# Kernel optimization log

Hardware: AMD Instinct MI355X
Metric: run time of the kernel (lower is better)

The kernel has to match this reference:

```python
import jax, jax.numpy as jnp
import numpy as np

B, L, H, HEADS, N_NODE = 1024, 200, 128, 8, 200000
MAXN = L + 1  # max_n_node
D = H // HEADS
EPS = 1e-12


def setup_inputs() -> dict:
    key = jax.random.key(0)
    ks = jax.random.split(key, 20)
    lengths = jax.random.randint(ks[0], (B,), 1, L + 1)
    mask = (jnp.arange(L)[None, :] < lengths[:, None]).astype(jnp.int32)  # contiguous 1s
    alias_inputs = jax.random.randint(ks[1], (B, L), 0, MAXN)
    items = jax.random.randint(ks[2], (B, MAXN), 0, N_NODE)

    def lin_w(k, o, i):
        return (jax.random.normal(k, (o, i), jnp.float32) * 0.1)

    inp = dict(
        alias_inputs=alias_inputs,
        items=items,
        mask=mask,
        emb_W=jax.random.normal(ks[3], (N_NODE, H), jnp.float32) * 0.1,
        # LastAttenion params
        W0=lin_w(ks[4], H, H), b0=jax.random.normal(ks[5], (H,), jnp.float32) * 0.1,
        W1=lin_w(ks[6], H, H), b1=jax.random.normal(ks[7], (H,), jnp.float32) * 0.1,
        W2=lin_w(ks[8], H, H), b2=jax.random.normal(ks[9], (H,), jnp.float32) * 0.1,
        # linear_q[0] (last_k = 1)
        Wq=lin_w(ks[10], H, H), bq=jax.random.normal(ks[11], (H,), jnp.float32) * 0.1,
        # linear_transform (2H -> H)
        Wt=lin_w(ks[12], H, 2 * H), bt=jax.random.normal(ks[13], (H,), jnp.float32) * 0.1,
        ln_g=jax.random.normal(ks[14], (H,), jnp.float32) * 0.1,
        ln_b=jax.random.normal(ks[15], (H,), jnp.float32) * 0.1,
    )
    return inp


def reference(alias_inputs, items, mask, emb_W, W0, b0, W1, b1, W2, b2, Wq, bq, Wt, bt, ln_g, ln_b):
    maskf = mask.astype(jnp.float32)
    # hidden = normalize(embedding(items)); dropout off (eval)
    hidden = emb_W[items]                                                  # [B, MAXN, H]
    hidden = hidden / (jnp.linalg.norm(hidden, axis=-1, keepdims=True) + EPS)
    # per-batch gather: seq_hidden[b, t] = hidden[b, alias_inputs[b, t]]
    seq = jnp.take_along_axis(hidden, alias_inputs[..., None], axis=1)     # [B, L, H]
    seq = seq * maskf[..., None]
    seq = seq / (jnp.linalg.norm(seq, axis=-1, keepdims=True) + EPS)
    # compute_scores
    lengths = mask.sum(1)
    last_idx = lengths - 1                                                 # >= 0 (lengths >= 1)
    ht_last = seq[jnp.arange(B), last_idx]                                 # [B, H]  (ht0 too)
    hts = (ht_last @ Wq.T + bq)[:, None, :]                                # [B, 1, H]
    # torch.norm over dim=1 (size 1) == elementwise abs
    hts = hts / (jnp.linalg.norm(hts, axis=1, keepdims=True) + EPS)
    # LastAttenion (last_k = 1, no lp-pool, eval dropout off)
    q0 = (hts @ W0.T + b0).reshape(B * HEADS, 1, D)                        # [B*h, 1, d]
    q1 = (seq @ W1.T + b1).reshape(B * HEADS, L, D)                        # [B*h, L, d]
    q2 = (seq @ W2.T + b2).reshape(B, L, HEADS, D)                         # [B, L, h, d]
    alpha = jax.nn.sigmoid(jnp.einsum('bkd,bld->bkl', q0, q1))             # [B*h, 1, L]
    alpha = alpha.reshape(B, HEADS, L).transpose(0, 2, 1)                  # [B, L, h]
    alpha = jax.nn.softmax(2.0 * alpha, axis=1)
    a = jnp.sum((alpha[..., None] * q2).reshape(B, L, H) * maskf[..., None], axis=1)  # [B, H]
    # layernorm eps=1e-8
    mu = a.mean(-1, keepdims=True)
    var = ((a - mu) ** 2).mean(-1, keepdims=True)
    a = (a - mu) / jnp.sqrt(var + 1e-8) * ln_g + ln_b
    a = jnp.concatenate([a, ht_last], axis=1) @ Wt.T + bt                  # [B, H]
    # norm=True branch
    a = a / (jnp.linalg.norm(a, axis=1, keepdims=True) + EPS)
    b = emb_W[1:]
    b = b / (jnp.linalg.norm(b, axis=1, keepdims=True) + EPS)
    return a, b.T                                                          # [B,H], [H, N_NODE-1]
```

## Files before the change

### kernel.cpp

```cpp
#include <hip/hip_runtime.h>
#include <math.h>

typedef unsigned int uint;
typedef unsigned short ushort;

__device__ __forceinline__ float b2f(ushort u){
  union { uint i; float f; } v; v.i = ((uint)u) << 16; return v.f;
}
__device__ __forceinline__ ushort f2b(float f){
  union { float f; uint i; } v; v.f = f;
  uint i = v.i;
  i += 0x7fffu + ((i >> 16) & 1u);
  return (ushort)(i >> 16);
}
__device__ __forceinline__ float wred(float v){
  #pragma unroll
  for (int s = 32; s > 0; s >>= 1) v += __shfl_xor(v, s, 64);
  return v;
}
__device__ __forceinline__ float gred16(float v){
  v += __shfl_xor(v, 1, 64);
  v += __shfl_xor(v, 2, 64);
  v += __shfl_xor(v, 4, 64);
  v += __shfl_xor(v, 8, 64);
  return v;
}
__device__ __forceinline__ float sane(float v){ return isfinite(v) ? v : 0.f; }
__device__ __forceinline__ int iclamp(int v, int lo, int hi){ return v < lo ? lo : (v > hi ? hi : v); }

__device__ __forceinline__ void load_raw8(const void* emb, int isf, int it, int p, float x[8]){
  if (it >= 0){
    if (isf){
      const float4* q = (const float4*)((const float*)emb + (size_t)it * 128);
      float4 u = q[p * 2], u2 = q[p * 2 + 1];
      x[0] = u.x; x[1] = u.y; x[2] = u.z; x[3] = u.w;
      x[4] = u2.x; x[5] = u2.y; x[6] = u2.z; x[7] = u2.w;
    } else {
      uint4 u = ((const uint4*)((const ushort*)emb + (size_t)it * 128))[p];
      x[0] = b2f((ushort)u.x); x[1] = b2f((ushort)(u.x >> 16));
      x[2] = b2f((ushort)u.y); x[3] = b2f((ushort)(u.y >> 16));
      x[4] = b2f((ushort)u.z); x[5] = b2f((ushort)(u.z >> 16));
      x[6] = b2f((ushort)u.w); x[7] = b2f((ushort)(u.w >> 16));
    }
  } else {
    #pragma unroll
    for (int e = 0; e < 8; ++e) x[e] = 0.f;
  }
}

#define OUTB 131072

#define C_W0T 0
#define C_W1  16384
#define C_W2T 32768
#define C_WQT 49152
#define C_WTT 65536
#define C_B0  98304
#define C_B1  98432
#define C_B2  98560
#define C_BQ  98688
#define C_BT  98816
#define C_G   98944
#define C_BB  99072
#define C_TOT 99200

#define KMAIN_SMEM 73984

__global__ __launch_bounds__(256) void k_detect(const ushort* __restrict__ emb,
                                                int* __restrict__ flag){
  __shared__ int s_bad;
  if (threadIdx.x == 0) s_bad = 0;
  __syncthreads();
  int bad = 0;
  for (int i = threadIdx.x; i < 8192; i += 256){
    float v = fabsf(b2f(emb[i]));
    if (!(v <= 1e4f)) bad = 1;
  }
  if (bad) s_bad = 1;
  __syncthreads();
  if (threadIdx.x == 0) flag[0] = s_bad;
}

__global__ __launch_bounds__(256) void k_wts(
    const void* W0, const void* b0, const void* W1, const void* b1,
    const void* W2, const void* b2, const void* Wq, const void* bq,
    const void* Wt, const void* bt, const void* g, const void* bb,
    const int* __restrict__ flag, float* __restrict__ wts){
  int j = blockIdx.x * 256 + threadIdx.x;
  if (j >= C_TOT) return;
  const int isf = flag[0];
  const void* src; int si;
  if (j < 16384)      { int k = j >> 7, h = j & 127; src = W0; si = h * 128 + k; }
  else if (j < 32768) { src = W1; si = j - 16384; }
  else if (j < 49152) { int i = j - 32768; int k = i >> 7, h = i & 127; src = W2; si = h * 128 + k; }
  else if (j < 65536) { int i = j - 49152; int k = i >> 7, h = i & 127; src = Wq; si = h * 128 + k; }
  else if (j < 98304) { int i = j - 65536; int k = i >> 7, h = i & 127; src = Wt; si = h * 256 + k; }
  else {
    int i = j - 98304; int arr = i >> 7;
    const void* tab[7] = { b0, b1, b2, bq, bt, g, bb };
    src = tab[arr]; si = i & 127;
  }
  wts[j] = isf ? ((const float*)src)[si] : b2f(((const ushort*)src)[si]);
}

__global__ __launch_bounds__(256) void k_bout(const void* __restrict__ emb,
                                              const int* __restrict__ flag,
                                              void* __restrict__ outv){
  __shared__ float tile[64 * 129];
  const int t = threadIdx.x, gid = t >> 4, p = t & 15;
  const int base = blockIdx.x * 64;
  const int isf = flag[0];
  for (int i = gid; i < 64; i += 16){
    int gi = base + i;
    if (gi < 199999){
      float x[8];
      if (isf){
        const float4* q = (const float4*)((const float*)emb + (size_t)(gi + 1) * 128);
        float4 u = q[p * 2], u2 = q[p * 2 + 1];
        x[0] = u.x; x[1] = u.y; x[2] = u.z; x[3] = u.w;
        x[4] = u2.x; x[5] = u2.y; x[6] = u2.z; x[7] = u2.w;
      } else {
        uint4 u = ((const uint4*)((const ushort*)emb + (size_t)(gi + 1) * 128))[p];
        x[0] = b2f((ushort)u.x); x[1] = b2f((ushort)(u.x >> 16));
        x[2] = b2f((ushort)u.y); x[3] = b2f((ushort)(u.y >> 16));
        x[4] = b2f((ushort)u.z); x[5] = b2f((ushort)(u.z >> 16));
        x[6] = b2f((ushort)u.w); x[7] = b2f((ushort)(u.w >> 16));
      }
      float ss = 0.f;
      #pragma unroll
      for (int e = 0; e < 8; ++e) ss += x[e] * x[e];
      ss = gred16(ss);
      float inv = 1.f / (sqrtf(ss) + 1e-12f);
      #pragma unroll
      for (int e = 0; e < 8; ++e) tile[i * 129 + p * 8 + e] = x[e] * inv;
    }
  }
  __syncthreads();
  for (int it = 0; it < 32; ++it){
    int idx = it * 256 + t;
    int h = idx >> 6, n = idx & 63;
    int gi = base + n;
    if (gi < 199999){
      float val = sane(tile[n * 129 + h]);
      if (isf) ((float*)outv)[OUTB + (size_t)h * 199999 + gi] = val;
      else     ((ushort*)outv)[OUTB + (size_t)h * 199999 + gi] = f2b(val);
    }
  }
}

__global__ __launch_bounds__(128) void k_prep(
    const int* __restrict__ alias_, const int* __restrict__ items,
    const int* __restrict__ mask, const void* __restrict__ emb,
    const float* __restrict__ wts, const int* __restrict__ flag,
    float* __restrict__ ws_ht, float* __restrict__ ws_X0,
    float* __restrict__ ws_c1, int* __restrict__ ws_len){
  __shared__ float s_ht[128], s_hts[128], s_X0s[128];
  __shared__ float s_red[8];
  __shared__ int s_item;
  const int b = blockIdx.x, t = threadIdx.x, w = t >> 6;
  const int isf = flag[0];

  int mv = mask[b * 200 + t] + (t < 72 ? mask[b * 200 + 128 + t] : 0);
  float lv = wred((float)mv);
  if ((t & 63) == 0) s_red[w] = lv;
  __syncthreads();
  int len = iclamp((int)(s_red[0] + s_red[1] + 0.5f), 1, 200);
  if (t == 0){
    ws_len[b] = len;
    int a = iclamp(alias_[b * 200 + len - 1], 0, 200);
    s_item = iclamp(items[b * 201 + a], 0, 199999);
  }
  __syncthreads();

  float v = isf ? ((const float*)emb)[(size_t)s_item * 128 + t]
                : b2f(((const ushort*)emb)[(size_t)s_item * 128 + t]);
  float ss = wred(v * v);
  if ((t & 63) == 0) s_red[2 + w] = ss;
  __syncthreads();
  v = v / (sqrtf(s_red[2] + s_red[3]) + 1e-12f);
  float ss2 = wred(v * v);
  if ((t & 63) == 0) s_red[4 + w] = ss2;
  __syncthreads();
  v = v / (sqrtf(s_red[4] + s_red[5]) + 1e-12f);
  s_ht[t] = v;
  ws_ht[b * 128 + t] = v;
  __syncthreads();

  {
    double acc = (double)wts[C_BQ + t];
    for (int k = 0; k < 128; ++k)
      acc += (double)wts[C_WQT + k * 128 + t] * (double)s_ht[k];
    float a = (float)acc;
    s_hts[t] = a / (fabsf(a) + 1e-12f);
  }
  __syncthreads();
  {
    float a0 = wts[C_B0 + t];
    for (int k = 0; k < 128; ++k) a0 += wts[C_W0T + k * 128 + t] * s_hts[k];
    s_X0s[t] = a0;
    ws_X0[b * 128 + t] = a0;
  }
  __syncthreads();
  if (t < 64){
    int head = t >> 3, j = t & 7;
    float c = 0.f;
    #pragma unroll
    for (int d = 0; d < 16; ++d) c += s_X0s[head * 16 + d] * wts[C_B1 + j * 16 + d];
    ws_c1[b * 64 + t] = c;
  }
}

__global__ __launch_bounds__(256) void k_main(
    const int* __restrict__ alias_, const int* __restrict__ items,
    const int* __restrict__ mask, const void* __restrict__ emb,
    const float* __restrict__ wts, const float* __restrict__ ws_ht,
    const float* __restrict__ ws_X0, const float* __restrict__ ws_c1,
    const int* __restrict__ ws_len, const int* __restrict__ flag,
    void* __restrict__ outv){
  extern __shared__ __align__(16) char dsm[];
  ushort* s_x     = (ushort*)dsm;
  ushort* s_w1p   = (ushort*)(dsm + 51200);
  float*  s_part  = (float*)(dsm + 51200);
  float*  s_alpha = (float*)(dsm + 51200 + 16384);

  __shared__ float s_X0[128], s_ht[128], s_a[128];
  __shared__ float s_c1[64];
  __shared__ float s_T[8], s_Tp[64];
  __shared__ float s_red[16];
  __shared__ int   s_it[200];

  const int b = blockIdx.x, t = threadIdx.x;
  const int wv = t >> 6, gid = t >> 4, p = t & 15, lane = t & 63;
  const int isf = flag[0];
  const int len = iclamp(ws_len[b], 1, 200);
  const int mbase = b * 200;

  if (t < 128){ s_X0[t] = ws_X0[b * 128 + t]; s_ht[t] = ws_ht[b * 128 + t]; }
  if (t < 64)  s_c1[t] = ws_c1[b * 64 + t];
  if (t < 200){
    int m = mask[mbase + t];
    int a = m ? iclamp(alias_[mbase + t], 0, 200) : 0;
    s_it[t] = m ? iclamp(items[b * 201 + a], 0, 199999) : -1;
  }
  __syncthreads();

  for (int idx = t; idx < 8192; idx += 256){
    int hj = idx >> 7, k = idx & 127, head = hj >> 3, j = hj & 7;
    float acc = 0.f;
    const float* w1r = wts + C_W1 + (j * 16) * 128 + k;
    #pragma unroll
    for (int d = 0; d < 16; ++d) acc += s_X0[head * 16 + d] * w1r[d * 128];
    s_w1p[hj * 128 + k] = f2b(acc);
  }
  __syncthreads();

  {
    float xc[8], xn[8];
    load_raw8(emb, isf, s_it[gid], p, xc);
    for (int r = gid; r < 200; r += 16){
      int rn = r + 16;
      load_raw8(emb, isf, rn < 200 ? s_it[rn] : -1, p, xn);

      float ss = 0.f;
      #pragma unroll
      for (int e = 0; e < 8; ++e) ss += xc[e] * xc[e];
      ss = gred16(ss);
      float inv = 1.f / (sqrtf(ss) + 1e-12f);
      #pragma unroll
      for (int e = 0; e < 8; ++e) xc[e] *= inv;

      uint4 u;
      u.x = (uint)f2b(xc[0]) | ((uint)f2b(xc[1]) << 16);
      u.y = (uint)f2b(xc[2]) | ((uint)f2b(xc[3]) << 16);
      u.z = (uint)f2b(xc[4]) | ((uint)f2b(xc[5]) << 16);
      u.w = (uint)f2b(xc[6]) | ((uint)f2b(xc[7]) << 16);
      *(uint4*)(s_x + r * 128 + p * 8) = u;

      int head = r / 25, lb = (r % 25) * 8;
      #pragma unroll
      for (int j = 0; j < 8; ++j){
        uint4 wu = *(const uint4*)(s_w1p + (head * 8 + j) * 128 + p * 8);
        float dot = xc[0] * b2f((ushort)wu.x) + xc[1] * b2f((ushort)(wu.x >> 16))
                  + xc[2] * b2f((ushort)wu.y) + xc[3] * b2f((ushort)(wu.y >> 16))
                  + xc[4] * b2f((ushort)wu.z) + xc[5] * b2f((ushort)(wu.z >> 16))
                  + xc[6] * b2f((ushort)wu.w) + xc[7] * b2f((ushort)(wu.w >> 16));
        dot = gred16(dot);
        if (p == 0){
          float logit = s_c1[head * 8 + j] + dot;
          s_alpha[(lb + j) * 8 + head] = 2.f / (1.f + expf(-logit));
        }
      }
      #pragma unroll
      for (int e = 0; e < 8; ++e) xc[e] = xn[e];
    }
  }
  __syncthreads();

  {
    int head = t >> 5, l32 = t & 31;
    float vals[7]; float mx = -1e30f;
    #pragma unroll
    for (int i = 0; i < 7; ++i){
      int l = l32 + 32 * i;
      float xx = (l < 200) ? s_alpha[l * 8 + head] : -1e30f;
      vals[i] = xx; mx = fmaxf(mx, xx);
    }
    #pragma unroll
    for (int s = 16; s > 0; s >>= 1) mx = fmaxf(mx, __shfl_xor(mx, s, 64));
    float sum = 0.f; float e[7];
    #pragma unroll
    for (int i = 0; i < 7; ++i){
      int l = l32 + 32 * i;
      float ex = (l < 200) ? expf(vals[i] - mx) : 0.f;
      e[i] = ex; sum += ex;
    }
    #pragma unroll
    for (int s = 16; s > 0; s >>= 1) sum += __shfl_xor(sum, s, 64);
    float inv = 1.f / sum;
    #pragma unroll
    for (int i = 0; i < 7; ++i){
      int l = l32 + 32 * i;
      if (l < 200) s_alpha[l * 8 + head] = e[i] * inv;
    }
  }
  __syncthreads();

  if (t < 64){
    int h = t & 7, seg = t >> 3;
    int l0 = seg * 25, l1 = l0 + 25; if (l1 > len) l1 = len;
    float s = 0.f;
    for (int l = l0; l < l1; ++l) s += s_alpha[l * 8 + h];
    s_Tp[t] = s;
  }
  __syncthreads();
  if (t < 8){
    float s = 0.f;
    #pragma unroll
    for (int seg = 0; seg < 8; ++seg) s += s_Tp[seg * 8 + t];
    s_T[t] = s;
  }

  float acc[64];
  #pragma unroll
  for (int e = 0; e < 64; ++e) acc[e] = 0.f;
  for (int l = gid; l < 200; l += 16){
    if (s_it[l] >= 0){
      uint4 xu = *(const uint4*)(s_x + l * 128 + p * 8);
      float x[8];
      x[0] = b2f((ushort)xu.x); x[1] = b2f((ushort)(xu.x >> 16));
      x[2] = b2f((ushort)xu.y); x[3] = b2f((ushort)(xu.y >> 16));
      x[4] = b2f((ushort)xu.z); x[5] = b2f((ushort)(xu.z >> 16));
      x[6] = b2f((ushort)xu.w); x[7] = b2f((ushort)(xu.w >> 16));
      float4 a0 = *(const float4*)(s_alpha + l * 8);
      float4 a1 = *(const float4*)(s_alpha + l * 8 + 4);
      float al[8] = { a0.x, a0.y, a0.z, a0.w, a1.x, a1.y, a1.z, a1.w };
      #pragma unroll
      for (int h = 0; h < 8; ++h)
        #pragma unroll
        for (int e = 0; e < 8; ++e) acc[h * 8 + e] += al[h] * x[e];
    }
  }
  #pragma unroll
  for (int e = 0; e < 64; ++e){
    float v = acc[e];
    v += __shfl_xor(v, 16, 64);
    v += __shfl_xor(v, 32, 64);
    acc[e] = v;
  }
  __syncthreads();
  if (lane < 16){
    #pragma unroll
    for (int h = 0; h < 8; ++h)
      #pragma unroll
      for (int e = 0; e < 8; ++e)
        s_part[wv * 1024 + h * 128 + p * 8 + e] = acc[h * 8 + e];
  }
  __syncthreads();
  for (int i = t; i < 1024; i += 256)
    s_part[i] = s_part[i] + s_part[1024 + i] + s_part[2048 + i] + s_part[3072 + i];
  __syncthreads();

  float araw = 0.f;
  if (t < 128){
    int head = t >> 4;
    araw = wts[C_B2 + t] * s_T[head];
    const float* hl = &s_part[head * 128];
    for (int k = 0; k < 128; ++k) araw += hl[k] * wts[C_W2T + k * 128 + t];
  }
  float v1 = wred(t < 128 ? araw : 0.f);
  if ((t & 63) == 0) s_red[t >> 6] = v1;
  __syncthreads();
  float mu = (s_red[0] + s_red[1]) * 0.0078125f;
  float dd = (t < 128) ? (araw - mu) : 0.f;
  float v2 = wred(dd * dd);
  if ((t & 63) == 0) s_red[4 + (t >> 6)] = v2;
  __syncthreads();
  float var = (s_red[4] + s_red[5]) * 0.0078125f;
  if (t < 128)
    s_a[t] = dd / sqrtf(var + 1e-8f) * wts[C_G + t] + wts[C_BB + t];
  __syncthreads();

  float o = 0.f;
  if (t < 128){
    o = wts[C_BT + t];
    for (int k = 0; k < 128; ++k) o += s_a[k] * wts[C_WTT + k * 128 + t];
    for (int k = 0; k < 128; ++k) o += s_ht[k] * wts[C_WTT + (128 + k) * 128 + t];
  }
  float v3 = wred(t < 128 ? o * o : 0.f);
  if ((t & 63) == 0) s_red[8 + (t >> 6)] = v3;
  __syncthreads();
  float nrm = sqrtf(s_red[8] + s_red[9]);
  if (t < 128){
    float val = sane(o / (nrm + 1e-12f));
    if (isf) ((float*)outv)[b * 128 + t] = val;
    else     ((ushort*)outv)[b * 128 + t] = f2b(val);
  }
}

extern "C" void kernel_launch(void* const* d_in, const int* in_sizes, int n_in,
                              void* d_out, int out_size, void* d_ws, size_t ws_size,
                              hipStream_t stream){
  const int* alias_ = (const int*)d_in[0];
  const int* items  = (const int*)d_in[1];
  const int* mask   = (const int*)d_in[2];
  const void* emb = d_in[3];
  const void* W0  = d_in[4];
  const void* b0  = d_in[5];
  const void* W1  = d_in[6];
  const void* b1  = d_in[7];
  const void* W2  = d_in[8];
  const void* b2_ = d_in[9];
  const void* Wq  = d_in[10];
  const void* bq  = d_in[11];
  const void* Wt  = d_in[12];
  const void* bt  = d_in[13];
  const void* g_  = d_in[14];
  const void* bb_ = d_in[15];

  char* ws = (char*)d_ws;
  int*   ws_flag = (int*)ws;
  float* wts     = (float*)(ws + 64);
  float* ws_ht   = (float*)(ws + 396864);
  float* ws_X0   = (float*)(ws + 921152);
  float* ws_c1   = (float*)(ws + 1445440);
  int*   ws_len  = (int*)(ws + 1707584);

  static int g_attr_done = 0;
  if (!g_attr_done){
    hipFuncSetAttribute(reinterpret_cast<const void*>(k_main),
                        hipFuncAttributeMaxDynamicSharedMemorySize, KMAIN_SMEM);
    g_attr_done = 1;
  }

  k_detect<<<dim3(1),    dim3(256), 0, stream>>>((const ushort*)emb, ws_flag);
  k_wts   <<<dim3(388),  dim3(256), 0, stream>>>(W0, b0, W1, b1, W2, b2_, Wq, bq,
                                                 Wt, bt, g_, bb_, ws_flag, wts);
  k_bout  <<<dim3(3125), dim3(256), 0, stream>>>(emb, ws_flag, d_out);
  k_prep  <<<dim3(1024), dim3(128), 0, stream>>>(alias_, items, mask, emb, wts, ws_flag,
                                                 ws_ht, ws_X0, ws_c1, ws_len);
  k_main  <<<dim3(1024), dim3(256), KMAIN_SMEM, stream>>>(alias_, items, mask, emb, wts,
                                                 ws_ht, ws_X0, ws_c1, ws_len, ws_flag, d_out);
}
```

Before: 409.5 us.

## Fuse detect, prep, bout and main kernels into one interleaved launch

Removes the separate dtype-detect kernel by having each block sample the embedding header itself. The prep stage is folded into the main per-batch block, so its intermediates stay in shared memory instead of going through a global workspace. The b-output transpose blocks are interleaved with main blocks in a single grid, one main block per four block IDs, so the memory-bound transpose overlaps the compute-heavy attention. In exchange, every block repeats a small detection read, and all bout blocks now reserve the larger main shared-memory allocation, which may reduce occupancy.

```diff
diff --git a/kernel.cpp b/kernel.cpp
--- a/kernel.cpp
+++ b/kernel.cpp
@@ -48,6 +48,25 @@
   }
 }
 
+__device__ __forceinline__ int detect_isf(const void* emb, int t, int* s_flag){
+  if (t == 0) *s_flag = 0;
+  __syncthreads();
+  if (t < 64){
+    uint4 u = ((const uint4*)emb)[t];
+    uint w[4] = { u.x, u.y, u.z, u.w };
+    int bad = 0;
+    #pragma unroll
+    for (int e = 0; e < 4; ++e){
+      float v0 = fabsf(b2f((ushort)w[e]));
+      float v1 = fabsf(b2f((ushort)(w[e] >> 16)));
+      if (!(v0 <= 1e4f) || !(v1 <= 1e4f)) bad = 1;
+    }
+    if (bad) *s_flag = 1;
+  }
+  __syncthreads();
+  return *s_flag;
+}
+
 #define OUTB 131072
 
 #define C_W0T 0
@@ -66,29 +85,21 @@
 
 #define KMAIN_SMEM 73984
 
-__global__ __launch_bounds__(256) void k_detect(const ushort* __restrict__ emb,
-                                                int* __restrict__ flag){
-  __shared__ int s_bad;
-  if (threadIdx.x == 0) s_bad = 0;
-  __syncthreads();
-  int bad = 0;
-  for (int i = threadIdx.x; i < 8192; i += 256){
-    float v = fabsf(b2f(emb[i]));
-    if (!(v <= 1e4f)) bad = 1;
-  }
-  if (bad) s_bad = 1;
-  __syncthreads();
-  if (threadIdx.x == 0) flag[0] = s_bad;
-}
+#define NB_MAIN 1024
+#define NB_BOUT 3125
+#define NB_TOT  4149
 
 __global__ __launch_bounds__(256) void k_wts(
+    const void* __restrict__ emb,
     const void* W0, const void* b0, const void* W1, const void* b1,
     const void* W2, const void* b2, const void* Wq, const void* bq,
     const void* Wt, const void* bt, const void* g, const void* bb,
-    const int* __restrict__ flag, float* __restrict__ wts){
-  int j = blockIdx.x * 256 + threadIdx.x;
+    float* __restrict__ wts){
+  __shared__ int s_flag;
+  const int t = threadIdx.x;
+  const int isf = detect_isf(emb, t, &s_flag);
+  int j = blockIdx.x * 256 + t;
   if (j >= C_TOT) return;
-  const int isf = flag[0];
   const void* src; int si;
   if (j < 16384)      { int k = j >> 7, h = j & 127; src = W0; si = h * 128 + k; }
   else if (j < 32768) { src = W1; si = j - 16384; }
@@ -103,13 +114,11 @@
   wts[j] = isf ? ((const float*)src)[si] : b2f(((const ushort*)src)[si]);
 }
 
-__global__ __launch_bounds__(256) void k_bout(const void* __restrict__ emb,
-                                              const int* __restrict__ flag,
-                                              void* __restrict__ outv){
-  __shared__ float tile[64 * 129];
-  const int t = threadIdx.x, gid = t >> 4, p = t & 15;
-  const int base = blockIdx.x * 64;
-  const int isf = flag[0];
+__device__ void bout_block(const void* __restrict__ emb, int isf,
+                           void* __restrict__ outv, int bb, int t, char* dsm){
+  float* tile = (float*)dsm;
+  const int gid = t >> 4, p = t & 15;
+  const int base = bb * 64;
   for (int i = gid; i < 64; i += 16){
     int gi = base + i;
     if (gi < 199999){
@@ -148,45 +157,71 @@
   }
 }
 
-__global__ __launch_bounds__(128) void k_prep(
+__global__ __launch_bounds__(256) void k_fused(
     const int* __restrict__ alias_, const int* __restrict__ items,
     const int* __restrict__ mask, const void* __restrict__ emb,
-    const float* __restrict__ wts, const int* __restrict__ flag,
-    float* __restrict__ ws_ht, float* __restrict__ ws_X0,
-    float* __restrict__ ws_c1, int* __restrict__ ws_len){
-  __shared__ float s_ht[128], s_hts[128], s_X0s[128];
-  __shared__ float s_red[8];
-  __shared__ int s_item;
-  const int b = blockIdx.x, t = threadIdx.x, w = t >> 6;
-  const int isf = flag[0];
-
-  int mv = mask[b * 200 + t] + (t < 72 ? mask[b * 200 + 128 + t] : 0);
+    const float* __restrict__ wts, void* __restrict__ outv){
+  extern __shared__ __align__(16) char dsm[];
+  __shared__ int s_flag;
+  __shared__ float s_X0[128], s_ht[128], s_a[128], s_hts[128];
+  __shared__ float s_c1[64];
+  __shared__ float s_T[8], s_Tp[64];
+  __shared__ float s_red[16];
+  __shared__ int   s_it[200];
+  __shared__ int   s_item;
+
+  const int t = threadIdx.x;
+  const int isf = detect_isf(emb, t, &s_flag);
+
+  const int bid = blockIdx.x;
+  const bool is_main = (bid < 4096) && ((bid & 3) == 0);
+  if (!is_main){
+    int bb = (bid < 4096) ? (bid - (bid >> 2) - 1) : (3072 + (bid - 4096));
+    bout_block(emb, isf, outv, bb, t, dsm);
+    return;
+  }
+  const int b = bid >> 2;
+
+  ushort* s_x     = (ushort*)dsm;
+  ushort* s_w1p   = (ushort*)(dsm + 51200);
+  float*  s_part  = (float*)(dsm + 51200);
+  float*  s_alpha = (float*)(dsm + 51200 + 16384);
+
+  const int wv = t >> 6, gid = t >> 4, p = t & 15, lane = t & 63;
+  const int mbase = b * 200;
+
+  int mv = 0;
+  if (t < 200){
+    mv = mask[mbase + t];
+    int a = mv ? iclamp(alias_[mbase + t], 0, 200) : 0;
+    s_it[t] = mv ? iclamp(items[b * 201 + a], 0, 199999) : -1;
+  }
   float lv = wred((float)mv);
-  if ((t & 63) == 0) s_red[w] = lv;
-  __syncthreads();
-  int len = iclamp((int)(s_red[0] + s_red[1] + 0.5f), 1, 200);
+  if ((t & 63) == 0) s_red[t >> 6] = lv;
+  __syncthreads();
+  const int len = iclamp((int)(s_red[0] + s_red[1] + s_red[2] + s_red[3] + 0.5f), 1, 200);
   if (t == 0){
-    ws_len[b] = len;
-    int a = iclamp(alias_[b * 200 + len - 1], 0, 200);
+    int a = iclamp(alias_[mbase + len - 1], 0, 200);
     s_item = iclamp(items[b * 201 + a], 0, 199999);
   }
   __syncthreads();
 
-  float v = isf ? ((const float*)emb)[(size_t)s_item * 128 + t]
-                : b2f(((const ushort*)emb)[(size_t)s_item * 128 + t]);
+  float v = 0.f;
+  if (t < 128)
+    v = isf ? ((const float*)emb)[(size_t)s_item * 128 + t]
+            : b2f(((const ushort*)emb)[(size_t)s_item * 128 + t]);
   float ss = wred(v * v);
-  if ((t & 63) == 0) s_red[2 + w] = ss;
-  __syncthreads();
-  v = v / (sqrtf(s_red[2] + s_red[3]) + 1e-12f);
+  if ((t & 63) == 0) s_red[4 + (t >> 6)] = ss;
+  __syncthreads();
+  v = v / (sqrtf(s_red[4] + s_red[5]) + 1e-12f);
   float ss2 = wred(v * v);
-  if ((t & 63) == 0) s_red[4 + w] = ss2;
-  __syncthreads();
-  v = v / (sqrtf(s_red[4] + s_red[5]) + 1e-12f);
-  s_ht[t] = v;
-  ws_ht[b * 128 + t] = v;
-  __syncthreads();
-
-  {
+  if ((t & 63) == 0) s_red[8 + (t >> 6)] = ss2;
+  __syncthreads();
+  v = v / (sqrtf(s_red[8] + s_red[9]) + 1e-12f);
+  if (t < 128) s_ht[t] = v;
+  __syncthreads();
+
+  if (t < 128){
     double acc = (double)wts[C_BQ + t];
     for (int k = 0; k < 128; ++k)
       acc += (double)wts[C_WQT + k * 128 + t] * (double)s_ht[k];
@@ -194,56 +229,21 @@
     s_hts[t] = a / (fabsf(a) + 1e-12f);
   }
   __syncthreads();
-  {
+  if (t < 128){
     float a0 = wts[C_B0 + t];
     for (int k = 0; k < 128; ++k) a0 += wts[C_W0T + k * 128 + t] * s_hts[k];
-    s_X0s[t] = a0;
-    ws_X0[b * 128 + t] = a0;
+    s_X0[t] = a0;
   }
   __syncthreads();
   if (t < 64){
     int head = t >> 3, j = t & 7;
     float c = 0.f;
     #pragma unroll
-    for (int d = 0; d < 16; ++d) c += s_X0s[head * 16 + d] * wts[C_B1 + j * 16 + d];
-    ws_c1[b * 64 + t] = c;
-  }
-}
-
-__global__ __launch_bounds__(256) void k_main(
-    const int* __restrict__ alias_, const int* __restrict__ items,
-    const int* __restrict__ mask, const void* __restrict__ emb,
-    const float* __restrict__ wts, const float* __restrict__ ws_ht,
-    const float* __restrict__ ws_X0, const float* __restrict__ ws_c1,
-    const int* __restrict__ ws_len, const int* __restrict__ flag,
-    void* __restrict__ outv){
-  extern __shared__ __align__(16) char dsm[];
-  ushort* s_x     = (ushort*)dsm;
-  ushort* s_w1p   = (ushort*)(dsm + 51200);
-  float*  s_part  = (float*)(dsm + 51200);
-  float*  s_alpha = (float*)(dsm + 51200 + 16384);
-
-  __shared__ float s_X0[128], s_ht[128], s_a[128];
-  __shared__ float s_c1[64];
-  __shared__ float s_T[8], s_Tp[64];
-  __shared__ float s_red[16];
-  __shared__ int   s_it[200];
-
-  const int b = blockIdx.x, t = threadIdx.x;
-  const int wv = t >> 6, gid = t >> 4, p = t & 15, lane = t & 63;
-  const int isf = flag[0];
-  const int len = iclamp(ws_len[b], 1, 200);
-  const int mbase = b * 200;
-
-  if (t < 128){ s_X0[t] = ws_X0[b * 128 + t]; s_ht[t] = ws_ht[b * 128 + t]; }
-  if (t < 64)  s_c1[t] = ws_c1[b * 64 + t];
-  if (t < 200){
-    int m = mask[mbase + t];
-    int a = m ? iclamp(alias_[mbase + t], 0, 200) : 0;
-    s_it[t] = m ? iclamp(items[b * 201 + a], 0, 199999) : -1;
-  }
-  __syncthreads();
-
+    for (int d = 0; d < 16; ++d) c += s_X0[head * 16 + d] * wts[C_B1 + j * 16 + d];
+    s_c1[t] = c;
+  }
+
+  __syncthreads();
   for (int idx = t; idx < 8192; idx += 256){
     int hj = idx >> 7, k = idx & 127, head = hj >> 3, j = hj & 7;
     float acc = 0.f;
@@ -261,11 +261,11 @@
       int rn = r + 16;
       load_raw8(emb, isf, rn < 200 ? s_it[rn] : -1, p, xn);
 
-      float ss = 0.f;
-      #pragma unroll
-      for (int e = 0; e < 8; ++e) ss += xc[e] * xc[e];
-      ss = gred16(ss);
-      float inv = 1.f / (sqrtf(ss) + 1e-12f);
+      float ssr = 0.f;
+      #pragma unroll
+      for (int e = 0; e < 8; ++e) ssr += xc[e] * xc[e];
+      ssr = gred16(ssr);
+      float inv = 1.f / (sqrtf(ssr) + 1e-12f);
       #pragma unroll
       for (int e = 0; e < 8; ++e) xc[e] *= inv;
 
@@ -362,10 +362,10 @@
   }
   #pragma unroll
   for (int e = 0; e < 64; ++e){
-    float v = acc[e];
-    v += __shfl_xor(v, 16, 64);
-    v += __shfl_xor(v, 32, 64);
-    acc[e] = v;
+    float vv = acc[e];
+    vv += __shfl_xor(vv, 16, 64);
+    vv += __shfl_xor(vv, 32, 64);
+    acc[e] = vv;
   }
   __syncthreads();
   if (lane < 16){
@@ -438,26 +438,17 @@
   const void* bb_ = d_in[15];
 
   char* ws = (char*)d_ws;
-  int*   ws_flag = (int*)ws;
-  float* wts     = (float*)(ws + 64);
-  float* ws_ht   = (float*)(ws + 396864);
-  float* ws_X0   = (float*)(ws + 921152);
-  float* ws_c1   = (float*)(ws + 1445440);
-  int*   ws_len  = (int*)(ws + 1707584);
+  float* wts = (float*)ws;
 
   static int g_attr_done = 0;
   if (!g_attr_done){
-    hipFuncSetAttribute(reinterpret_cast<const void*>(k_main),
+    hipFuncSetAttribute(reinterpret_cast<const void*>(k_fused),
                         hipFuncAttributeMaxDynamicSharedMemorySize, KMAIN_SMEM);
     g_attr_done = 1;
   }
 
-  k_detect<<<dim3(1),    dim3(256), 0, stream>>>((const ushort*)emb, ws_flag);
-  k_wts   <<<dim3(388),  dim3(256), 0, stream>>>(W0, b0, W1, b1, W2, b2_, Wq, bq,
-                                                 Wt, bt, g_, bb_, ws_flag, wts);
-  k_bout  <<<dim3(3125), dim3(256), 0, stream>>>(emb, ws_flag, d_out);
-  k_prep  <<<dim3(1024), dim3(128), 0, stream>>>(alias_, items, mask, emb, wts, ws_flag,
-                                                 ws_ht, ws_X0, ws_c1, ws_len);
-  k_main  <<<dim3(1024), dim3(256), KMAIN_SMEM, stream>>>(alias_, items, mask, emb, wts,
-                                                 ws_ht, ws_X0, ws_c1, ws_len, ws_flag, d_out);
-}
+  k_wts  <<<dim3(388),     dim3(256), 0,          stream>>>(emb, W0, b0, W1, b1,
+                                                  W2, b2_, Wq, bq, Wt, bt, g_, bb_, wts);
+  k_fused<<<dim3(NB_TOT),  dim3(256), KMAIN_SMEM, stream>>>(alias_, items, mask, emb,
+                                                  wts, d_out);
+}
```

After: 757.4 us. 84.9% more time.
